# Performance work log

Hardware: AMD Instinct MI355X
Metric: run time of the kernel (lower is better)

The kernel has to match this reference:

```python
import jax, jax.numpy as jnp
import numpy as np

GAMMA = 0.5          # cfg.distribution_loss.triplet_loss_gamma
POS_RADIUS = 0.6     # cfg.fine_loss.positive_radius
BIG = 1e12

B, K = 4096, 64      # node correspondences, knn points per node
N = K + 1            # matching_scores has one slack row/col


def setup_inputs() -> dict:
    key = jax.random.key(0)
    k1, k2, k3, k4, k5 = jax.random.split(key, 5)
    pos_pts = jax.random.normal(k1, (B, K, 3), dtype=jnp.float32)
    # anchor points near positives so some pairs fall inside positive_radius
    anc_pts = pos_pts + 0.3 * jax.random.normal(k2, (B, K, 3), dtype=jnp.float32)
    pos_masks = jax.random.uniform(k3, (B, K)) < 0.9
    anc_masks = jax.random.uniform(k4, (B, K)) < 0.9
    matching_scores = jax.random.normal(k5, (B, N, N), dtype=jnp.float32)
    transform = jnp.eye(4, dtype=jnp.float32)  # rigid SE(3); identity keeps pos/neg masks realistic
    return {
        'pos_node_corr_knn_points': pos_pts,
        'anc_node_corr_knn_points': anc_pts,
        'pos_node_corr_knn_masks': pos_masks,
        'anc_node_corr_knn_masks': anc_masks,
        'matching_scores': matching_scores,
        'transform': transform,
    }


def _apply_transform(points, transform):
    R = transform[:3, :3]
    t = transform[:3, 3]
    return jnp.einsum('bkd,ed->bke', points, R) + t


def _pairwise_sq_dist(x, y):
    # (b,n,3),(b,m,3) -> (b,n,m) squared distances
    x2 = jnp.sum(x * x, axis=-1)
    y2 = jnp.sum(y * y, axis=-1)
    xy = jnp.einsum('bnd,bmd->bnm', x, y)
    return x2[:, :, None] - 2.0 * xy + y2[:, None, :]


def reference(pos_node_corr_knn_points, anc_node_corr_knn_points,
              pos_node_corr_knn_masks, anc_node_corr_knn_masks,
              matching_scores, transform):
    b, n, m = matching_scores.shape
    anc = _apply_transform(anc_node_corr_knn_points, transform)
    dists = _pairwise_sq_dist(pos_node_corr_knn_points, anc)  # (b, n-1, m-1)

    gt_masks = pos_node_corr_knn_masks[:, :, None] & anc_node_corr_knn_masks[:, None, :]
    gt_corr = (dists < POS_RADIUS ** 2) & gt_masks
    gt_neg = dists > (2.0 * POS_RADIUS) ** 2
    row_none = jnp.sum(gt_corr, axis=2) == 0   # (b, n-1): rows w/o correspondence -> slack col
    col_none = jnp.sum(gt_corr, axis=1) == 0   # (b, m-1): cols w/o correspondence -> slack row

    pos_mask = (jnp.zeros((b, n, m), dtype=bool)
                .at[:, :-1, :-1].set(gt_corr)
                .at[:, :-1, -1].set(row_none)
                .at[:, -1, :-1].set(col_none))
    neg_mask = (jnp.zeros((b, n, m), dtype=bool)
                .at[:, :-1, :-1].set(gt_neg)
                .at[:, :-1, -1].set(~row_none)
                .at[:, -1, :-1].set(~col_none))

    ms = matching_scores

    # ---- row direction (over pos knn rows, all m cols) ----
    pm = pos_mask[:, :-1, :]
    nm = neg_mask[:, :-1, :]
    ms_r = ms[:, :-1, :]
    pos_score = jnp.sum(jnp.where(pm, -ms_r, 0.0), axis=2) / jnp.sum(pm, axis=2)  # (b, n-1); count>=1
    neg_score = jnp.where(nm, -ms_r, BIG)                                          # (b, n-1, m)
    gap1 = pos_score[:, :, None] - neg_score
    per1 = jnp.log(jnp.sum(jnp.maximum(gap1 + GAMMA, 0.0), axis=2) + 1.0)          # (b, n-1)
    keep1 = pos_score != BIG
    loss1 = jnp.sum(jnp.where(keep1, per1, 0.0)) / jnp.maximum(jnp.sum(keep1), 1)

    # ---- column direction (over anc knn cols, all n rows) ----
    pmc = pos_mask[:, :, :-1]
    nmc = neg_mask[:, :, :-1]
    ms_c = ms[:, :, :-1]
    pos_score_inv = jnp.sum(jnp.where(pmc, -ms_c, 0.0), axis=1) / jnp.sum(pmc, axis=1)  # (b, m-1)
    neg_score_inv = jnp.where(nmc, -ms_c, BIG)                                           # (b, n, m-1)
    gap2 = jnp.transpose(pos_score_inv[:, None, :] - neg_score_inv, (0, 2, 1))           # (b, m-1, n)
    per2 = jnp.log(jnp.sum(jnp.maximum(gap2 + GAMMA, 0.0), axis=2) + 1.0)                # (b, m-1)
    keep2 = pos_score_inv != BIG
    loss2 = jnp.sum(jnp.where(keep2, per2, 0.0)) / jnp.maximum(jnp.sum(keep2), 1)

    return (loss1 + loss2) / 2.0
```

## Files before the change

### kernel.cpp

```cpp
#include <hip/hip_runtime.h>
#include <hip/hip_fp16.h>


#define R2_POS 0.36f
#define R2_NEG 1.44f
#define GAMMA_C 0.5f
#define NBATCH 4096
#define NPART (NBATCH * 2)

__device__ __forceinline__ int maskbit(const void* p, int i, int mode) {
    if (mode == 0) return ((const unsigned*)p)[i] != 0u;
    if (mode == 1) return ((const unsigned short*)p)[i] != 0;
    return ((const unsigned char*)p)[i] != 0;
}

__global__ __launch_bounds__(128, 8)
void fused_kernel(const float* __restrict__ posp,
                  const float* __restrict__ ancp,
                  const void* __restrict__ pmp,
                  const void* __restrict__ amp,
                  const float* __restrict__ msp,
                  const float* __restrict__ xfp,
                  float* __restrict__ partials) {
    __shared__ __half2 tile2[2114];
    __shared__ float4 ancs[64];
    __shared__ float4 poss[64];

    const int tid = threadIdx.x;
    const int b = blockIdx.x;
    const int w = tid >> 6;
    const int l = tid & 63;
    const int ofs = b & 1;

    unsigned mw0 = ((const unsigned*)pmp)[l];
    bool okw = (mw0 == 0u) || (mw0 == 1u) || (mw0 == 0x3F800000u);
    unsigned hh0 = mw0 & 0xFFFFu, hh1 = mw0 >> 16;
    bool okh = (hh0 == 0u || hh0 == 0x3F80u) && (hh1 == 0u || hh1 == 0x3F80u);
    int mmode = (__ballot(okw) == ~0ULL) ? 0 : ((__ballot(okh) == ~0ULL) ? 1 : 2);

    float T[12];
#pragma unroll
    for (int e = 0; e < 3; ++e)
#pragma unroll
        for (int d = 0; d < 4; ++d) T[e * 4 + d] = xfp[e * 4 + d];

    const int pb = (b * 64 + l) * 3;
    const float px = posp[pb], py = posp[pb + 1], pz = posp[pb + 2];
    const float r0 = ancp[pb], r1 = ancp[pb + 1], r2 = ancp[pb + 2];
    const float ax = T[0] * r0 + T[1] * r1 + T[2]  * r2 + T[3];
    const float ay = T[4] * r0 + T[5] * r1 + T[6]  * r2 + T[7];
    const float az = T[8] * r0 + T[9] * r1 + T[10] * r2 + T[11];

    const int mi = b * 64 + l;
    const unsigned long long pmM = __ballot(maskbit(pmp, mi, mmode) != 0);
    const unsigned long long amM = __ballot(maskbit(amp, mi, mmode) != 0);

    if (w == 0) ancs[l] = make_float4(ax, ay, az, 0.f);
    else        poss[l] = make_float4(px, py, pz, 0.f);

    {
        const float2* src = (const float2*)(msp + (size_t)b * 4225 - ofs);
#pragma unroll
        for (int k = 0; k < 17; ++k) {
            int idx = tid + 128 * k;
            if (idx < 2113) tile2[idx] = __float22half2_rn(src[idx]);
        }
    }
    __syncthreads();

    const __half* t = ((const __half*)tile2) + ofs;
    float result;

    if (w == 0) {
        const __half* row = t + l * 65;
        const bool pmL = (pmM >> l) & 1ULL;
        float psum = 0.f; int pcnt = 0;
        unsigned nlo = 0u, nhi = 0u;
#pragma unroll 16
        for (int j = 0; j < 64; ++j) {
            float v = __half2float(row[j]);
            float4 a = ancs[j];
            float dx = px - a.x, dy = py - a.y, dz = pz - a.z;
            float d2 = dx * dx + dy * dy + dz * dz;
            bool pos = pmL && ((amM >> j) & 1ULL) && (d2 < R2_POS);
            if (pos) { psum -= v; pcnt++; }
            bool neg = d2 > R2_NEG;
            if (j < 32) nlo |= (neg ? (1u << j) : 0u);
            else        nhi |= (neg ? (1u << (j - 32)) : 0u);
        }
        const float slack = __half2float(row[64]);
        const float ps = pcnt ? psum / (float)pcnt : -slack;
        float hv = 0.f;
#pragma unroll 16
        for (int j = 0; j < 32; ++j)
            if ((nlo >> j) & 1u) hv += fmaxf(ps + __half2float(row[j]) + GAMMA_C, 0.f);
#pragma unroll 16
        for (int j = 32; j < 64; ++j)
            if ((nhi >> (j - 32)) & 1u) hv += fmaxf(ps + __half2float(row[j]) + GAMMA_C, 0.f);
        if (pcnt) hv += fmaxf(ps + slack + GAMMA_C, 0.f);
        result = __logf(hv + 1.f);
    } else {
        const bool amL = (amM >> l) & 1ULL;
        float psum = 0.f; int pcnt = 0;
        unsigned nlo = 0u, nhi = 0u;
#pragma unroll 16
        for (int r = 0; r < 64; ++r) {
            float v = __half2float(t[r * 65 + l]);
            float4 p = poss[r];
            float dx = p.x - ax, dy = p.y - ay, dz = p.z - az;
            float d2 = dx * dx + dy * dy + dz * dz;
            bool pos = ((pmM >> r) & 1ULL) && amL && (d2 < R2_POS);
            if (pos) { psum -= v; pcnt++; }
            bool neg = d2 > R2_NEG;
            if (r < 32) nlo |= (neg ? (1u << r) : 0u);
            else        nhi |= (neg ? (1u << (r - 32)) : 0u);
        }
        const float slack = __half2float(t[64 * 65 + l]);
        const float ps = pcnt ? psum / (float)pcnt : -slack;
        float hv = 0.f;
#pragma unroll 16
        for (int r = 0; r < 32; ++r)
            if ((nlo >> r) & 1u) hv += fmaxf(ps + __half2float(t[r * 65 + l]) + GAMMA_C, 0.f);
#pragma unroll 16
        for (int r = 32; r < 64; ++r)
            if ((nhi >> (r - 32)) & 1u) hv += fmaxf(ps + __half2float(t[r * 65 + l]) + GAMMA_C, 0.f);
        if (pcnt) hv += fmaxf(ps + slack + GAMMA_C, 0.f);
        result = __logf(hv + 1.f);
    }

#pragma unroll
    for (int off = 1; off < 64; off <<= 1)
        result += __shfl_xor(result, off, 64);
    if (l == 0) partials[b * 2 + w] = result;

}

__global__ void finalize_kernel(const float* __restrict__ partials,
                                unsigned* __restrict__ out) {
    __shared__ float red[4];
    const int tid = threadIdx.x;
    float s = 0.f;
    for (int i = tid; i < NPART; i += 256) s += partials[i];
#pragma unroll
    for (int off = 1; off < 64; off <<= 1) s += __shfl_xor(s, off, 64);
    if ((tid & 63) == 0) red[tid >> 6] = s;
    __syncthreads();
    if (tid == 0) {
        float tot = red[0] + red[1] + red[2] + red[3];
        float loss = tot * (1.0f / (2.0f * NBATCH * 64.0f));
        unsigned bits = __float_as_uint(loss);
        unsigned h = (bits + 0x7FFFu + ((bits >> 16) & 1u)) >> 16;
        out[0] = (h << 16) | h;
    }
}

extern "C" void kernel_launch(void* const* d_in, const int* in_sizes, int n_in,
                              void* d_out, int out_size, void* d_ws, size_t ws_size,
                              hipStream_t stream) {
    (void)in_sizes; (void)n_in; (void)out_size; (void)ws_size;
    const float* posp = (const float*)d_in[0];
    const float* ancp = (const float*)d_in[1];
    const void* pmp = d_in[2];
    const void* amp = d_in[3];
    const float* msp = (const float*)d_in[4];
    const float* xfp = (const float*)d_in[5];

    fused_kernel<<<NBATCH, 128, 0, stream>>>(posp, ancp, pmp, amp, msp, xfp,
                                             (float*)d_ws);
    finalize_kernel<<<1, 256, 0, stream>>>((const float*)d_ws,
                                           (unsigned*)d_out);
}
```

Measured before the change: 148.8 us.

## Cache masked scores in packed half registers and read column scores from global

Each lane now stores its 64 row or column scores in registers as packed fp16 pairs during the distance pass. Non-negative entries are replaced by a large negative sentinel, so the hinge sum becomes a branchless packed-half add/max loop with no second LDS pass. The column wave now reads matching scores and positive points directly from global memory instead of the shared tile and a shared positions array, so the poss buffer is removed. The tile fill is restructured into paired float2 loads, and the occupancy hint drops from 8 to 7 to accommodate the larger register footprint. The hinge sum is now accumulated in fp16, which costs accuracy, and the strided global reads for the column wave may add memory latency.

Result: faster. 138.3 us (-7.1%).

```diff
diff --git a/kernel.cpp b/kernel.cpp
--- a/kernel.cpp
+++ b/kernel.cpp
@@ -7,6 +7,9 @@
 #define GAMMA_C 0.5f
 #define NBATCH 4096
 #define NPART (NBATCH * 2)
+#define HCNEG -1024.0f
+
+typedef _Float16 hf2 __attribute__((ext_vector_type(2)));
 
 __device__ __forceinline__ int maskbit(const void* p, int i, int mode) {
     if (mode == 0) return ((const unsigned*)p)[i] != 0u;
@@ -14,7 +17,7 @@
     return ((const unsigned char*)p)[i] != 0;
 }
 
-__global__ __launch_bounds__(128, 8)
+__global__ __launch_bounds__(128, 7)
 void fused_kernel(const float* __restrict__ posp,
                   const float* __restrict__ ancp,
                   const void* __restrict__ pmp,
@@ -24,7 +27,6 @@
                   float* __restrict__ partials) {
     __shared__ __half2 tile2[2114];
     __shared__ float4 ancs[64];
-    __shared__ float4 poss[64];
 
     const int tid = threadIdx.x;
     const int b = blockIdx.x;
@@ -56,83 +58,98 @@
     const unsigned long long amM = __ballot(maskbit(amp, mi, mmode) != 0);
 
     if (w == 0) ancs[l] = make_float4(ax, ay, az, 0.f);
-    else        poss[l] = make_float4(px, py, pz, 0.f);
 
     {
         const float2* src = (const float2*)(msp + (size_t)b * 4225 - ofs);
 #pragma unroll
-        for (int k = 0; k < 17; ++k) {
-            int idx = tid + 128 * k;
-            if (idx < 2113) tile2[idx] = __float22half2_rn(src[idx]);
+        for (int k = 0; k < 8; ++k) {
+            int idx = 2 * tid + 256 * k;
+            float2 a = src[idx], c = src[idx + 1];
+            tile2[idx]     = __float22half2_rn(a);
+            tile2[idx + 1] = __float22half2_rn(c);
+        }
+        int idx = 2048 + 2 * tid;
+        if (idx < 2112) {
+            float2 a = src[idx], c = src[idx + 1];
+            tile2[idx]     = __float22half2_rn(a);
+            tile2[idx + 1] = __float22half2_rn(c);
+        } else if (idx == 2112) {
+            tile2[idx] = __float22half2_rn(src[idx]);
         }
     }
     __syncthreads();
 
-    const __half* t = ((const __half*)tile2) + ofs;
-    float result;
+    float psum = 0.f; int pcnt = 0; float slack;
+    hf2 hc[32];
 
     if (w == 0) {
-        const __half* row = t + l * 65;
+        const __half* row = ((const __half*)tile2) + ofs + l * 65;
         const bool pmL = (pmM >> l) & 1ULL;
-        float psum = 0.f; int pcnt = 0;
-        unsigned nlo = 0u, nhi = 0u;
-#pragma unroll 16
-        for (int j = 0; j < 64; ++j) {
-            float v = __half2float(row[j]);
-            float4 a = ancs[j];
-            float dx = px - a.x, dy = py - a.y, dz = pz - a.z;
-            float d2 = dx * dx + dy * dy + dz * dz;
-            bool pos = pmL && ((amM >> j) & 1ULL) && (d2 < R2_POS);
-            if (pos) { psum -= v; pcnt++; }
-            bool neg = d2 > R2_NEG;
-            if (j < 32) nlo |= (neg ? (1u << j) : 0u);
-            else        nhi |= (neg ? (1u << (j - 32)) : 0u);
+#pragma unroll
+        for (int jj = 0; jj < 32; ++jj) {
+            float h0, h1;
+#pragma unroll
+            for (int s = 0; s < 2; ++s) {
+                const int j = 2 * jj + s;
+                float v = __half2float(row[j]);
+                float4 a = ancs[j];
+                float dx = px - a.x, dy = py - a.y, dz = pz - a.z;
+                float d2 = dx * dx + dy * dy + dz * dz;
+                bool pos = pmL && ((amM >> j) & 1ULL) && (d2 < R2_POS);
+                psum -= pos ? v : 0.f;
+                pcnt += pos ? 1 : 0;
+                float hcv = (d2 > R2_NEG) ? v : HCNEG;
+                if (s == 0) h0 = hcv; else h1 = hcv;
+            }
+            hf2 h; h[0] = (_Float16)h0; h[1] = (_Float16)h1;
+            hc[jj] = h;
         }
-        const float slack = __half2float(row[64]);
-        const float ps = pcnt ? psum / (float)pcnt : -slack;
-        float hv = 0.f;
-#pragma unroll 16
-        for (int j = 0; j < 32; ++j)
-            if ((nlo >> j) & 1u) hv += fmaxf(ps + __half2float(row[j]) + GAMMA_C, 0.f);
-#pragma unroll 16
-        for (int j = 32; j < 64; ++j)
-            if ((nhi >> (j - 32)) & 1u) hv += fmaxf(ps + __half2float(row[j]) + GAMMA_C, 0.f);
-        if (pcnt) hv += fmaxf(ps + slack + GAMMA_C, 0.f);
-        result = __logf(hv + 1.f);
+        slack = __half2float(row[64]);
     } else {
+        const float* mcol = msp + (size_t)b * 4225 + l;
         const bool amL = (amM >> l) & 1ULL;
-        float psum = 0.f; int pcnt = 0;
-        unsigned nlo = 0u, nhi = 0u;
-#pragma unroll 16
-        for (int r = 0; r < 64; ++r) {
-            float v = __half2float(t[r * 65 + l]);
-            float4 p = poss[r];
-            float dx = p.x - ax, dy = p.y - ay, dz = p.z - az;
-            float d2 = dx * dx + dy * dy + dz * dz;
-            bool pos = ((pmM >> r) & 1ULL) && amL && (d2 < R2_POS);
-            if (pos) { psum -= v; pcnt++; }
-            bool neg = d2 > R2_NEG;
-            if (r < 32) nlo |= (neg ? (1u << r) : 0u);
-            else        nhi |= (neg ? (1u << (r - 32)) : 0u);
+#pragma unroll
+        for (int jj = 0; jj < 32; ++jj) {
+            float h0, h1;
+#pragma unroll
+            for (int s = 0; s < 2; ++s) {
+                const int r = 2 * jj + s;
+                float v = mcol[r * 65];
+                const int qb = (b * 64 + r) * 3;
+                float qx = posp[qb], qy = posp[qb + 1], qz = posp[qb + 2];
+                float dx = qx - ax, dy = qy - ay, dz = qz - az;
+                float d2 = dx * dx + dy * dy + dz * dz;
+                bool pos = ((pmM >> r) & 1ULL) && amL && (d2 < R2_POS);
+                psum -= pos ? v : 0.f;
+                pcnt += pos ? 1 : 0;
+                float hcv = (d2 > R2_NEG) ? v : HCNEG;
+                if (s == 0) h0 = hcv; else h1 = hcv;
+            }
+            hf2 h; h[0] = (_Float16)h0; h[1] = (_Float16)h1;
+            hc[jj] = h;
         }
-        const float slack = __half2float(t[64 * 65 + l]);
-        const float ps = pcnt ? psum / (float)pcnt : -slack;
-        float hv = 0.f;
-#pragma unroll 16
-        for (int r = 0; r < 32; ++r)
-            if ((nlo >> r) & 1u) hv += fmaxf(ps + __half2float(t[r * 65 + l]) + GAMMA_C, 0.f);
-#pragma unroll 16
-        for (int r = 32; r < 64; ++r)
-            if ((nhi >> (r - 32)) & 1u) hv += fmaxf(ps + __half2float(t[r * 65 + l]) + GAMMA_C, 0.f);
-        if (pcnt) hv += fmaxf(ps + slack + GAMMA_C, 0.f);
-        result = __logf(hv + 1.f);
+        slack = mcol[64 * 65];
     }
+
+    const float ps = pcnt ? psum / (float)pcnt : -slack;
+
+    const _Float16 ch = (_Float16)(ps + GAMMA_C);
+    const hf2 C2 = {ch, ch};
+    const hf2 Z = {(_Float16)0.f, (_Float16)0.f};
+    float hv = 0.f;
+#pragma unroll
+    for (int k = 0; k < 32; ++k) {
+        hf2 x = hc[k] + C2;
+        x = __builtin_elementwise_max(x, Z);
+        hv += (float)x[0] + (float)x[1];
+    }
+    if (pcnt) hv += fmaxf(ps + slack + GAMMA_C, 0.f);
+    float result = __logf(hv + 1.f);
 
 #pragma unroll
     for (int off = 1; off < 64; off <<= 1)
         result += __shfl_xor(result, off, 64);
     if (l == 0) partials[b * 2 + w] = result;
-
 }
 
 __global__ void finalize_kernel(const float* __restrict__ partials,
```

## Double-buffer score tiles via global_load_lds across four batches per block

Applied to the files above, without the earlier changes.

Each block now handles four batches and stages the next batch's score tile straight into LDS with global_load_lds while computing the current one. Tiles stay fp32 instead of being converted to half, and the next batch's points and masks are loaded ahead. This aims to hide global load latency and cut the block count. In exchange LDS per block roughly doubles, which limits occupancy, and there is a per-batch sync. The code does not wait explicitly for the asynchronous LDS loads before the barrier, which may be a correctness risk.

New measurement: 162.6 us. +9.3%, slower.

```diff
diff --git a/kernel.cpp b/kernel.cpp
--- a/kernel.cpp
+++ b/kernel.cpp
@@ -1,5 +1,4 @@
 #include <hip/hip_runtime.h>
-#include <hip/hip_fp16.h>
 
 
 #define R2_POS 0.36f
@@ -8,13 +7,21 @@
 #define NBATCH 4096
 #define NPART (NBATCH * 2)
 
+#define AS1 __attribute__((address_space(1)))
+#define AS3 __attribute__((address_space(3)))
+
+__device__ __forceinline__ void dma_dword(const float* g, float* lds) {
+    __builtin_amdgcn_global_load_lds((const AS1 void*)g, (AS3 void*)lds,
+                                     4, 0, 0);
+}
+
 __device__ __forceinline__ int maskbit(const void* p, int i, int mode) {
     if (mode == 0) return ((const unsigned*)p)[i] != 0u;
     if (mode == 1) return ((const unsigned short*)p)[i] != 0;
     return ((const unsigned char*)p)[i] != 0;
 }
 
-__global__ __launch_bounds__(128, 8)
+__global__ __launch_bounds__(128)
 void fused_kernel(const float* __restrict__ posp,
                   const float* __restrict__ ancp,
                   const void* __restrict__ pmp,
@@ -22,15 +29,14 @@
                   const float* __restrict__ msp,
                   const float* __restrict__ xfp,
                   float* __restrict__ partials) {
-    __shared__ __half2 tile2[2114];
-    __shared__ float4 ancs[64];
-    __shared__ float4 poss[64];
+    __shared__ float tiles[2][4225];
+    __shared__ float4 ancs[2][64];
+    __shared__ float4 poss[2][64];
 
     const int tid = threadIdx.x;
-    const int b = blockIdx.x;
     const int w = tid >> 6;
     const int l = tid & 63;
-    const int ofs = b & 1;
+    const int bb = blockIdx.x * 4;
 
     unsigned mw0 = ((const unsigned*)pmp)[l];
     bool okw = (mw0 == 0u) || (mw0 == 1u) || (mw0 == 0x3F800000u);
@@ -44,95 +50,125 @@
 #pragma unroll
         for (int d = 0; d < 4; ++d) T[e * 4 + d] = xfp[e * 4 + d];
 
-    const int pb = (b * 64 + l) * 3;
-    const float px = posp[pb], py = posp[pb + 1], pz = posp[pb + 2];
-    const float r0 = ancp[pb], r1 = ancp[pb + 1], r2 = ancp[pb + 2];
-    const float ax = T[0] * r0 + T[1] * r1 + T[2]  * r2 + T[3];
-    const float ay = T[4] * r0 + T[5] * r1 + T[6]  * r2 + T[7];
-    const float az = T[8] * r0 + T[9] * r1 + T[10] * r2 + T[11];
-
-    const int mi = b * 64 + l;
-    const unsigned long long pmM = __ballot(maskbit(pmp, mi, mmode) != 0);
-    const unsigned long long amM = __ballot(maskbit(amp, mi, mmode) != 0);
-
-    if (w == 0) ancs[l] = make_float4(ax, ay, az, 0.f);
-    else        poss[l] = make_float4(px, py, pz, 0.f);
-
-    {
-        const float2* src = (const float2*)(msp + (size_t)b * 4225 - ofs);
-#pragma unroll
-        for (int k = 0; k < 17; ++k) {
-            int idx = tid + 128 * k;
-            if (idx < 2113) tile2[idx] = __float22half2_rn(src[idx]);
+    float px, py, pz, ax, ay, az;
+    float npx, npy, npz, nax, nay, naz;
+    int mpv, mav, nmpv, nmav;
+
+#define LOADPTS(batch, PX, PY, PZ, AX, AY, AZ, MP, MA)                       \
+    {                                                                        \
+        const int pb = ((batch) * 64 + l) * 3;                               \
+        PX = posp[pb]; PY = posp[pb + 1]; PZ = posp[pb + 2];                 \
+        float r0 = ancp[pb], r1 = ancp[pb + 1], r2 = ancp[pb + 2];           \
+        AX = T[0] * r0 + T[1] * r1 + T[2]  * r2 + T[3];                      \
+        AY = T[4] * r0 + T[5] * r1 + T[6]  * r2 + T[7];                      \
+        AZ = T[8] * r0 + T[9] * r1 + T[10] * r2 + T[11];                     \
+        MP = maskbit(pmp, (batch) * 64 + l, mmode);                          \
+        MA = maskbit(amp, (batch) * 64 + l, mmode);                          \
+    }
+
+#define STAGE(buf, batch)                                                    \
+    {                                                                        \
+        const float* g = msp + (size_t)(batch) * 4225;                       \
+        float* d = tiles[buf];                                               \
+        for (int c = w; c <= 66; c += 2) {                                   \
+            int idx = c * 64 + l;                                            \
+            if (idx < 4225) dma_dword(g + idx, d + c * 64);                  \
+        }                                                                    \
+    }
+
+    STAGE(0, bb);
+    LOADPTS(bb, px, py, pz, ax, ay, az, mpv, mav);
+    if (w == 0) ancs[0][l] = make_float4(ax, ay, az, 0.f);
+    else        poss[0][l] = make_float4(px, py, pz, 0.f);
+    unsigned long long pmM = __ballot(mpv != 0);
+    unsigned long long amM = __ballot(mav != 0);
+    __syncthreads();
+
+    for (int i = 0; i < 4; ++i) {
+        const int cur = i & 1, nxt = cur ^ 1;
+        const int batch = bb + i;
+
+        if (i < 3) {
+            STAGE(nxt, batch + 1);
+            LOADPTS(batch + 1, npx, npy, npz, nax, nay, naz, nmpv, nmav);
         }
-    }
-    __syncthreads();
-
-    const __half* t = ((const __half*)tile2) + ofs;
-    float result;
-
-    if (w == 0) {
-        const __half* row = t + l * 65;
-        const bool pmL = (pmM >> l) & 1ULL;
+
         float psum = 0.f; int pcnt = 0;
         unsigned nlo = 0u, nhi = 0u;
-#pragma unroll 16
-        for (int j = 0; j < 64; ++j) {
-            float v = __half2float(row[j]);
-            float4 a = ancs[j];
-            float dx = px - a.x, dy = py - a.y, dz = pz - a.z;
-            float d2 = dx * dx + dy * dy + dz * dz;
-            bool pos = pmL && ((amM >> j) & 1ULL) && (d2 < R2_POS);
-            if (pos) { psum -= v; pcnt++; }
-            bool neg = d2 > R2_NEG;
-            if (j < 32) nlo |= (neg ? (1u << j) : 0u);
-            else        nhi |= (neg ? (1u << (j - 32)) : 0u);
+        float slack, hv = 0.f;
+
+        if (w == 0) {
+            const float* row = tiles[cur] + l * 65;
+            const float4* A = ancs[cur];
+            const bool pmL = (pmM >> l) & 1ULL;
+#pragma unroll 16
+            for (int j = 0; j < 64; ++j) {
+                float4 a = A[j];
+                float dx = px - a.x, dy = py - a.y, dz = pz - a.z;
+                float d2 = dx * dx + dy * dy + dz * dz;
+                float v = row[j];
+                bool pos = pmL && ((amM >> j) & 1ULL) && (d2 < R2_POS);
+                psum -= pos ? v : 0.f;
+                pcnt += pos ? 1 : 0;
+                bool neg = d2 > R2_NEG;
+                if (j < 32) nlo |= neg ? (1u << j) : 0u;
+                else        nhi |= neg ? (1u << (j - 32)) : 0u;
+            }
+            slack = row[64];
+            const float ps = pcnt ? psum / (float)pcnt : -slack;
+            const float c = ps + GAMMA_C;
+#pragma unroll 16
+            for (int j = 0; j < 32; ++j)
+                if ((nlo >> j) & 1u) hv += fmaxf(c + row[j], 0.f);
+#pragma unroll 16
+            for (int j = 32; j < 64; ++j)
+                if ((nhi >> (j - 32)) & 1u) hv += fmaxf(c + row[j], 0.f);
+            if (pcnt) hv += fmaxf(c + slack, 0.f);
+        } else {
+            const float* t = tiles[cur];
+            const float4* P = poss[cur];
+            const bool amL = (amM >> l) & 1ULL;
+#pragma unroll 16
+            for (int r = 0; r < 64; ++r) {
+                float4 p = P[r];
+                float dx = p.x - ax, dy = p.y - ay, dz = p.z - az;
+                float d2 = dx * dx + dy * dy + dz * dz;
+                float v = t[r * 65 + l];
+                bool pos = ((pmM >> r) & 1ULL) && amL && (d2 < R2_POS);
+                psum -= pos ? v : 0.f;
+                pcnt += pos ? 1 : 0;
+                bool neg = d2 > R2_NEG;
+                if (r < 32) nlo |= neg ? (1u << r) : 0u;
+                else        nhi |= neg ? (1u << (r - 32)) : 0u;
+            }
+            slack = t[64 * 65 + l];
+            const float ps = pcnt ? psum / (float)pcnt : -slack;
+            const float c = ps + GAMMA_C;
+#pragma unroll 16
+            for (int r = 0; r < 32; ++r)
+                if ((nlo >> r) & 1u) hv += fmaxf(c + t[r * 65 + l], 0.f);
+#pragma unroll 16
+            for (int r = 32; r < 64; ++r)
+                if ((nhi >> (r - 32)) & 1u) hv += fmaxf(c + t[r * 65 + l], 0.f);
+            if (pcnt) hv += fmaxf(c + slack, 0.f);
         }
-        const float slack = __half2float(row[64]);
-        const float ps = pcnt ? psum / (float)pcnt : -slack;
-        float hv = 0.f;
-#pragma unroll 16
-        for (int j = 0; j < 32; ++j)
-            if ((nlo >> j) & 1u) hv += fmaxf(ps + __half2float(row[j]) + GAMMA_C, 0.f);
-#pragma unroll 16
-        for (int j = 32; j < 64; ++j)
-            if ((nhi >> (j - 32)) & 1u) hv += fmaxf(ps + __half2float(row[j]) + GAMMA_C, 0.f);
-        if (pcnt) hv += fmaxf(ps + slack + GAMMA_C, 0.f);
-        result = __logf(hv + 1.f);
-    } else {
-        const bool amL = (amM >> l) & 1ULL;
-        float psum = 0.f; int pcnt = 0;
-        unsigned nlo = 0u, nhi = 0u;
-#pragma unroll 16
-        for (int r = 0; r < 64; ++r) {
-            float v = __half2float(t[r * 65 + l]);
-            float4 p = poss[r];
-            float dx = p.x - ax, dy = p.y - ay, dz = p.z - az;
-            float d2 = dx * dx + dy * dy + dz * dz;
-            bool pos = ((pmM >> r) & 1ULL) && amL && (d2 < R2_POS);
-            if (pos) { psum -= v; pcnt++; }
-            bool neg = d2 > R2_NEG;
-            if (r < 32) nlo |= (neg ? (1u << r) : 0u);
-            else        nhi |= (neg ? (1u << (r - 32)) : 0u);
+
+        float result = __logf(hv + 1.f);
+#pragma unroll
+        for (int off = 1; off < 64; off <<= 1)
+            result += __shfl_xor(result, off, 64);
+        if (l == 0) partials[batch * 2 + w] = result;
+
+        if (i < 3) {
+            px = npx; py = npy; pz = npz;
+            ax = nax; ay = nay; az = naz;
+            if (w == 0) ancs[nxt][l] = make_float4(ax, ay, az, 0.f);
+            else        poss[nxt][l] = make_float4(px, py, pz, 0.f);
+            pmM = __ballot(nmpv != 0);
+            amM = __ballot(nmav != 0);
         }
-        const float slack = __half2float(t[64 * 65 + l]);
-        const float ps = pcnt ? psum / (float)pcnt : -slack;
-        float hv = 0.f;
-#pragma unroll 16
-        for (int r = 0; r < 32; ++r)
-            if ((nlo >> r) & 1u) hv += fmaxf(ps + __half2float(t[r * 65 + l]) + GAMMA_C, 0.f);
-#pragma unroll 16
-        for (int r = 32; r < 64; ++r)
-            if ((nhi >> (r - 32)) & 1u) hv += fmaxf(ps + __half2float(t[r * 65 + l]) + GAMMA_C, 0.f);
-        if (pcnt) hv += fmaxf(ps + slack + GAMMA_C, 0.f);
-        result = __logf(hv + 1.f);
-    }
-
-#pragma unroll
-    for (int off = 1; off < 64; off <<= 1)
-        result += __shfl_xor(result, off, 64);
-    if (l == 0) partials[b * 2 + w] = result;
-
+        __syncthreads();
+    }
 }
 
 __global__ void finalize_kernel(const float* __restrict__ partials,
@@ -165,8 +201,8 @@
     const float* msp = (const float*)d_in[4];
     const float* xfp = (const float*)d_in[5];
 
-    fused_kernel<<<NBATCH, 128, 0, stream>>>(posp, ancp, pmp, amp, msp, xfp,
-                                             (float*)d_ws);
+    fused_kernel<<<NBATCH / 4, 128, 0, stream>>>(posp, ancp, pmp, amp, msp,
+                                                 xfp, (float*)d_ws);
     finalize_kernel<<<1, 256, 0, stream>>>((const float*)d_ws,
                                            (unsigned*)d_out);
 }
```
